# Kernel optimization log

Measured on AMD Instinct MI355X. Metric: run time of the kernel, lower is better.

Reference implementation:

```python
import jax, jax.numpy as jnp
import numpy as np

NQ, NS, QN, SN = 10000, 500, 4, 10   # num_question, num_skill, q/s neighbor sizes
B, S, D = 32, 200, 128               # batch, seq_len, emb_dim
HOPS = 3


def setup_inputs() -> dict:
    key = jax.random.key(0)
    ks = iter(jax.random.split(key, 40))

    def nrm(shape, scale=0.05):
        return jax.random.normal(next(ks), shape, dtype=jnp.float32) * scale

    return {
        "question": jax.random.randint(next(ks), (B, S), 0, NQ),
        "response": jax.random.randint(next(ks), (B, S), 0, 2),
        "mask": jnp.ones((B, S), dtype=jnp.int32),
        "q_neighbors": jax.random.randint(next(ks), (NQ, QN), 0, NS),  # question -> skill ids
        "s_neighbors": jax.random.randint(next(ks), (NS, SN), 0, NQ),  # skill -> question ids
        "qs_skills": jax.random.randint(next(ks), (NQ, 4), 0, NS),     # related skills per question
        "emb_q": nrm((NQ, D), 1.0),
        "emb_s": nrm((NS, D), 1.0),
        "emb_r": nrm((2, D), 1.0),
        "W_ih": nrm((2 * D, 4 * D)), "b_ih": nrm((4 * D,)), "b_hh": nrm((4 * D,)),
        "ft_W": nrm((D, D)), "ft_b": nrm((D,)),
        "agg_W": nrm((HOPS, D, D)), "agg_b": nrm((HOPS, D)),
        "last_W": nrm((D, D)), "last_b": nrm((D,)),
        "q_W": nrm((D, D)), "q_b": nrm((D,)),
        "k_W": nrm((D, D)), "k_b": nrm((D,)),
        "w_W": nrm((2 * D,)), "w_b": nrm(()),
    }


def reference(question, response, mask, q_neighbors, s_neighbors, qs_skills,
              emb_q, emb_s, emb_r, W_ih, b_ih, b_hh, ft_W, ft_b,
              agg_W, agg_b, last_W, last_b, q_W, q_b, k_W, k_b, w_W, w_b):
    # ---- multi-hop GNN aggregation for every (b, t) question (mask == 1 everywhere) ----
    q_flat = question.reshape(-1)              # [B*S]
    lvl1 = q_neighbors[q_flat]                 # [N, QN]            skill ids
    lvl2 = s_neighbors[lvl1]                   # [N, QN, SN]        question ids
    lvl3 = q_neighbors[lvl2]                   # [N, QN, SN, QN]    skill ids
    embs = [emb_q[q_flat], emb_s[lvl1], emb_q[lvl2], emb_s[lvl3]]
    for i in range(HOPS):
        embs = [jnp.tanh((embs[j] + embs[j + 1].mean(axis=-2)) @ agg_W[j] + agg_b[j])
                for j in range(HOPS - i)]
    agg_emb = jnp.tanh(embs[0] @ last_W + last_b).reshape(B, S, D)

    # ---- per-step input + zero-state LSTMCell (source calls lstm_cell without hx) ----
    q_trans = jax.nn.relu(agg_emb @ ft_W + ft_b)
    x = jnp.concatenate([q_trans, emb_r[response]], axis=-1)   # [B, S, 2D]
    gates = x @ W_ih + b_ih + b_hh                             # h_prev = 0, c_prev = 0
    i_g, f_g, g_g, o_g = jnp.split(gates, 4, axis=-1)
    c = jax.nn.sigmoid(i_g) * jnp.tanh(g_g)
    h = jax.nn.sigmoid(o_g) * jnp.tanh(c)                      # [B, S, D]
    states = h[:, :S - 1]                                      # state written at step t

    # ---- soft-recap attention prediction for q_next = question[:, t+1] ----
    q_next = question[:, 1:]                                   # [B, T], T = S-1
    qs = jnp.concatenate([emb_q[q_next][:, :, None, :], emb_s[qs_skills[q_next]]], axis=2)  # [B,T,5,D]

    inner = jnp.einsum('bnd,btmd->btnm', states, qs)           # state/qs inner products
    a_state = (states @ q_W + q_b) @ w_W[:D]                   # [B, N]  MLP_query on states
    a_qs = (qs @ k_W + k_b) @ w_W[D:]                          # [B, T, 5] MLP_key on qs
    logits = a_state[:, None, :, None] + a_qs[:, :, None, :] + w_b  # [B, T, N, 5]

    t_idx = jnp.arange(S - 1)
    valid = t_idx[None, :] <= t_idx[:, None]                   # [T, N]: states 0..t visible at t
    logits = jnp.where(valid[None, :, :, None], logits, -jnp.inf)
    alpha = jax.nn.softmax(logits.reshape(B, S - 1, -1), axis=-1).reshape(logits.shape)
    pred = jnp.sum(alpha * jax.nn.sigmoid(inner), axis=(2, 3))  # [B, T]

    return jnp.zeros((B, S), jnp.float32).at[:, 1:].set(pred)
```

## Files before the change

### kernel.cpp

```cpp
#include <hip/hip_runtime.h>

typedef unsigned short u16;
typedef unsigned int   u32;

#define NQd 10000
#define NSd 500
#define Bd  32
#define Sd  200
#define Td  199
#define Dd  128
#define NR  6368

typedef __attribute__((ext_vector_type(8))) short bf16x8;
typedef __attribute__((ext_vector_type(4))) float f32x4;

__device__ __forceinline__ float sigf(float x) { return 1.f / (1.f + __expf(-x)); }
__device__ __forceinline__ float bf2f(u16 u) { return __uint_as_float(((u32)u) << 16); }
__device__ __forceinline__ u16 f2bf(float f) {
  u32 b = __float_as_uint(f);
  b += 0x7FFFu + ((b >> 16) & 1u);
  return (u16)(b >> 16);
}
__device__ __forceinline__ void unp2(u32 u, float &a, float &b) {
  a = __uint_as_float(u << 16);
  b = __uint_as_float(u & 0xffff0000u);
}
__device__ __forceinline__ void unpack16(uint4 a0, uint4 a1, float* f) {
  unp2(a0.x, f[0], f[1]);  unp2(a0.y, f[2], f[3]);
  unp2(a0.z, f[4], f[5]);  unp2(a0.w, f[6], f[7]);
  unp2(a1.x, f[8], f[9]);  unp2(a1.y, f[10], f[11]);
  unp2(a1.z, f[12], f[13]); unp2(a1.w, f[14], f[15]);
}

struct Args {
  const int *question, *response, *q_nb, *s_nb, *qs_sk;
  const float *emb_q, *emb_s, *emb_r;
  const float *W_ih, *b_ih, *b_hh, *ft_W, *ft_b, *agg_W, *agg_b, *last_W, *last_b;
  const float *q_W, *q_b, *k_W, *k_b, *w_W;
  u16 *tabA, *tabB, *tabC, *tabs1, *tabs2, *G, *states, *embq_bf, *embs_bf, *wts, *wiht;
  float *a_state, *qw, *kw, *scal, *er_part;
  int *qid_map, *resp_map;
};

#define SMEM_U16 21760

__device__ __forceinline__ void mfma_accum(const u16* Al, const u16* Wl,
                                           int l15, int quad, int cw, f32x4 acc[2][2])
{
#pragma unroll
  for (int kc = 0; kc < 4; ++kc) {
    const int ko = kc * 32 + quad * 8;
    bf16x8 af[2], bfv[2];
    af[0]  = *(const bf16x8*)&Al[l15 * 136 + ko];
    af[1]  = *(const bf16x8*)&Al[(16 + l15) * 136 + ko];
    bfv[0] = *(const bf16x8*)&Wl[(cw + l15) * 136 + ko];
    bfv[1] = *(const bf16x8*)&Wl[(cw + 16 + l15) * 136 + ko];
#pragma unroll
    for (int mt = 0; mt < 2; ++mt)
#pragma unroll
      for (int nt = 0; nt < 2; ++nt)
        acc[mt][nt] = __builtin_amdgcn_mfma_f32_16x16x32_bf16(af[mt], bfv[nt], acc[mt][nt], 0, 0, 0);
  }
}

__device__ __forceinline__ void zero_acc(f32x4 acc[2][2]) {
#pragma unroll
  for (int x = 0; x < 2; ++x)
#pragma unroll
    for (int y = 0; y < 2; ++y) acc[x][y] = (f32x4){0.f, 0.f, 0.f, 0.f};
}

__device__ __forceinline__ void stage_A(const u16* Atab, const u16* Btab,
                                        const int* nbr, int K, int tile0, int rows,
                                        int tid, u16* Al)
{
  int r = tid & 31, k0 = (tid >> 5) * 16;
  int row = tile0 + r; if (row >= rows) row = rows - 1;
  const u16* ap = Atab + (long)row * 128 + k0;
  if (K == 0) {
    *(uint4*)&Al[r * 136 + k0]     = *(const uint4*)ap;
    *(uint4*)&Al[r * 136 + k0 + 8] = *(const uint4*)(ap + 8);
  } else {
    float f[16];
    unpack16(*(const uint4*)ap, *(const uint4*)(ap + 8), f);
    float s[16];
#pragma unroll
    for (int q = 0; q < 16; ++q) s[q] = 0.f;
    for (int l = 0; l < K; ++l) {
      int id = nbr[(long)row * K + l];
      const u16* np = Btab + (long)id * 128 + k0;
      float g[16];
      unpack16(*(const uint4*)np, *(const uint4*)(np + 8), g);
#pragma unroll
      for (int q = 0; q < 16; ++q) s[q] += g[q];
    }
    float inv = 1.f / (float)K;
#pragma unroll
    for (int q = 0; q < 16; ++q) f[q] += s[q] * inv;
    u32 p[8];
#pragma unroll
    for (int q = 0; q < 8; ++q)
      p[q] = (u32)f2bf(f[2 * q]) | ((u32)f2bf(f[2 * q + 1]) << 16);
    *(uint4*)&Al[r * 136 + k0]     = make_uint4(p[0], p[1], p[2], p[3]);
    *(uint4*)&Al[r * 136 + k0 + 8] = make_uint4(p[4], p[5], p[6], p[7]);
  }
}

__device__ __forceinline__ void stage_W(const u16* Wt, int tid, u16* Wl)
{
  for (int i = tid; i < 2048; i += 256) {
    int col = i >> 4, seg = i & 15;
    *(uint4*)&Wl[col * 136 + seg * 8] = *(const uint4*)&Wt[(long)col * 128 + seg * 8];
  }
}

__device__ __forceinline__ void gemm_tile(
    const u16* __restrict__ Atab, const u16* __restrict__ Btab,
    const int* __restrict__ nbr, int K,
    const u16* __restrict__ Wt, const float* __restrict__ cbias,
    u16* __restrict__ out, int rows, int tile0, int tid, u16* smem)
{
  u16* Wl = smem;
  u16* Al = smem + 17408;
  stage_W(Wt, tid, Wl);
  stage_A(Atab, Btab, nbr, K, tile0, rows, tid, Al);
  __syncthreads();
  const int lane = tid & 63, wv = tid >> 6;
  const int l15 = lane & 15, quad = lane >> 4, cw = wv * 32;
  f32x4 acc[2][2];
  zero_acc(acc);
  mfma_accum(Al, Wl, l15, quad, cw, acc);
#pragma unroll
  for (int nt = 0; nt < 2; ++nt) {
    int col = cw + nt * 16 + l15;
    float cb = cbias[col];
#pragma unroll
    for (int mt = 0; mt < 2; ++mt) {
      int rbase = tile0 + mt * 16 + quad * 4;
#pragma unroll
      for (int i = 0; i < 4; ++i) {
        int row = rbase + i;
        if (row >= rows) continue;
        out[(long)row * 128 + col] = f2bf(tanhf(acc[mt][nt][i] + cb));
      }
    }
  }
}

__global__ __launch_bounds__(256) void prep_all(Args a)
{
  const int T = gridDim.x * 256;
  for (int i = blockIdx.x * 256 + threadIdx.x; i < 491106; i += T) {
    if (i < 320000) {
      float4 v = *(const float4*)&a.emb_q[(long)i * 4];
      ((uint2*)a.embq_bf)[i] = make_uint2(
          (u32)f2bf(v.x) | ((u32)f2bf(v.y) << 16),
          (u32)f2bf(v.z) | ((u32)f2bf(v.w) << 16));
    } else if (i < 336000) {
      int c = i - 320000;
      float4 v = *(const float4*)&a.emb_s[(long)c * 4];
      ((uint2*)a.embs_bf)[c] = make_uint2(
          (u32)f2bf(v.x) | ((u32)f2bf(v.y) << 16),
          (u32)f2bf(v.z) | ((u32)f2bf(v.w) << 16));
    } else if (i < 417920) {
      int e = i - 336000;
      int seg = e >> 14, r = e & 16383;
      int col = r >> 7, k = r & 127;
      const float* src = (seg < 3) ? (a.agg_W + seg * 16384)
                                   : (seg == 3 ? a.last_W : a.ft_W);
      a.wts[e] = f2bf(src[k * 128 + col]);
    } else if (i < 483456) {
      int e = i - 417920;
      int col = e >> 7, k = e & 127;
      a.wiht[e] = f2bf(a.W_ih[k * 512 + col]);
    } else if (i < 489824) {
      int j = i - 483456;
      int b = j / Td, s = j - b * Td;
      a.qid_map[j]  = a.question[b * Sd + s];
      a.resp_map[j] = a.response[b * Sd + s];
    } else {
      int s = i - 489824;
      if (s < 128) {
        float acc = 0;
        for (int e = 0; e < 128; ++e) acc += a.q_W[s * 128 + e] * a.w_W[e];
        a.qw[s] = acc;
      } else if (s < 256) {
        int d = s - 128; float acc = 0;
        for (int e = 0; e < 128; ++e) acc += a.k_W[d * 128 + e] * a.w_W[128 + e];
        a.kw[d] = acc;
      } else if (s == 256) {
        float acc = 0;
        for (int e = 0; e < 128; ++e) acc += a.q_b[e] * a.w_W[e];
        a.scal[0] = acc;
      } else if (s == 257) {
        float acc = 0;
        for (int e = 0; e < 128; ++e) acc += a.k_b[e] * a.w_W[128 + e];
        a.scal[1] = acc;
      } else {
        int e2 = s - 258, rr = e2 >> 9, col = e2 & 511;
        float acc = a.b_ih[col] + a.b_hh[col];
        for (int d = 0; d < 128; ++d) acc += a.emb_r[rr * Dd + d] * a.W_ih[(128 + d) * 512 + col];
        a.er_part[rr * 512 + col] = acc;
      }
    }
  }
}

__global__ __launch_bounds__(256) void level1(Args a)
{
  __shared__ __align__(16) u16 smem[SMEM_U16];
  const int i = blockIdx.x, tid = threadIdx.x;
  if (i < 313)
    gemm_tile(a.embq_bf, a.embs_bf, a.q_nb, 4, a.wts + 2 * 16384,
              a.agg_b + 256, a.tabA, NQd, i * 32, tid, smem);
  else if (i < 329)
    gemm_tile(a.embs_bf, a.embq_bf, a.s_nb, 10, a.wts + 16384,
              a.agg_b + 128, a.tabs1, NSd, (i - 313) * 32, tid, smem);
  else
    gemm_tile(a.embq_bf, a.embs_bf, a.q_nb, 4, a.wts,
              a.agg_b, a.tabB, NQd, (i - 329) * 32, tid, smem);
}

__global__ __launch_bounds__(256) void level2(Args a)
{
  __shared__ __align__(16) u16 smem[SMEM_U16];
  const int i = blockIdx.x, tid = threadIdx.x;
  if (i < 16)
    gemm_tile(a.tabs1, a.tabA, a.s_nb, 10, a.wts + 16384,
              a.agg_b + 128, a.tabs2, NSd, i * 32, tid, smem);
  else
    gemm_tile(a.tabB, a.tabs1, a.q_nb, 4, a.wts,
              a.agg_b, a.tabC, NQd, (i - 16) * 32, tid, smem);
}

__global__ __launch_bounds__(256) void chain3(Args a)
{
  __shared__ __align__(16) u16 smem[SMEM_U16];
  u16* Wl = smem;
  u16* Al = smem + 17408;
  const int tid = threadIdx.x;
  const int tile0 = blockIdx.x * 32;
  const int lane = tid & 63, wv = tid >> 6;
  const int l15 = lane & 15, quad = lane >> 4, cw = wv * 32;
  f32x4 acc[2][2];

  stage_W(a.wts, tid, Wl);
  stage_A(a.tabC, a.tabs2, a.q_nb, 4, tile0, NQd, tid, Al);
  __syncthreads();
  zero_acc(acc);
  mfma_accum(Al, Wl, l15, quad, cw, acc);
  __syncthreads();
#pragma unroll
  for (int nt = 0; nt < 2; ++nt) {
    int col = cw + nt * 16 + l15;
    float cb = a.agg_b[col];
#pragma unroll
    for (int mt = 0; mt < 2; ++mt)
#pragma unroll
      for (int i = 0; i < 4; ++i) {
        int rL = mt * 16 + quad * 4 + i;
        Al[rL * 136 + col] = f2bf(tanhf(acc[mt][nt][i] + cb));
      }
  }
  stage_W(a.wts + 3 * 16384, tid, Wl);
  __syncthreads();

  zero_acc(acc);
  mfma_accum(Al, Wl, l15, quad, cw, acc);
  __syncthreads();
#pragma unroll
  for (int nt = 0; nt < 2; ++nt) {
    int col = cw + nt * 16 + l15;
    float cb = a.last_b[col];
#pragma unroll
    for (int mt = 0; mt < 2; ++mt)
#pragma unroll
      for (int i = 0; i < 4; ++i) {
        int rL = mt * 16 + quad * 4 + i;
        Al[rL * 136 + col] = f2bf(tanhf(acc[mt][nt][i] + cb));
      }
  }
  stage_W(a.wts + 4 * 16384, tid, Wl);
  __syncthreads();

  zero_acc(acc);
  mfma_accum(Al, Wl, l15, quad, cw, acc);
#pragma unroll
  for (int nt = 0; nt < 2; ++nt) {
    int col = cw + nt * 16 + l15;
    float cb = a.ft_b[col];
#pragma unroll
    for (int mt = 0; mt < 2; ++mt) {
      int rbase = tile0 + mt * 16 + quad * 4;
#pragma unroll
      for (int i = 0; i < 4; ++i) {
        int row = rbase + i;
        if (row >= NQd) continue;
        a.tabA[(long)row * 128 + col] = f2bf(fmaxf(acc[mt][nt][i] + cb, 0.f));
      }
    }
  }
}

__global__ __launch_bounds__(256) void gates_k(Args a)
{
  __shared__ __align__(16) u16 smem[SMEM_U16];
  u16* Wl = smem;
  u16* Al = smem + 17408;
  const int tid = threadIdx.x;
  const int tile0 = blockIdx.x * 32;
  {
    int r = tid & 31, k0 = (tid >> 5) * 16;
    int row = tile0 + r;
    int arow = a.qid_map[row];
    const u16* ap = a.tabA + (long)arow * 128 + k0;
    *(uint4*)&Al[r * 136 + k0]     = *(const uint4*)ap;
    *(uint4*)&Al[r * 136 + k0 + 8] = *(const uint4*)(ap + 8);
  }
  const int lane = tid & 63, wv = tid >> 6;
  const int l15 = lane & 15, quad = lane >> 4, cw = wv * 32;
  f32x4 acc[3][2][2];
  const int goff[3] = {0, 256, 384};
#pragma unroll
  for (int p = 0; p < 3; ++p) {
    __syncthreads();
    stage_W(a.wiht + (long)goff[p] * 128, tid, Wl);
    __syncthreads();
    zero_acc(acc[p]);
    mfma_accum(Al, Wl, l15, quad, cw, acc[p]);
  }
  __syncthreads();
  float* hb = (float*)Wl;
#pragma unroll
  for (int nt = 0; nt < 2; ++nt) {
    int colL = cw + nt * 16 + l15;
#pragma unroll
    for (int mt = 0; mt < 2; ++mt) {
#pragma unroll
      for (int i = 0; i < 4; ++i) {
        int rL = mt * 16 + quad * 4 + i;
        int row = tile0 + rL;
        const float* rb = a.er_part + (long)a.resp_map[row] * 512;
        float iv = acc[0][mt][nt][i] + rb[colL];
        float gv = acc[1][mt][nt][i] + rb[256 + colL];
        float ov = acc[2][mt][nt][i] + rb[384 + colL];
        float c = sigf(iv) * tanhf(gv);
        float h = sigf(ov) * tanhf(c);
        a.states[(long)row * 128 + colL] = f2bf(h);
        hb[rL * 132 + colL] = h;
      }
    }
  }
  __syncthreads();
#pragma unroll
  for (int rr = 0; rr < 8; ++rr) {
    int rL = wv * 8 + rr;
    float p = hb[rL * 132 + lane] * a.qw[lane] + hb[rL * 132 + 64 + lane] * a.qw[64 + lane];
#pragma unroll
    for (int off = 32; off > 0; off >>= 1) p += __shfl_xor(p, off);
    if (lane == 0) a.a_state[tile0 + rL] = p + a.scal[0];
  }
}

__global__ __launch_bounds__(256) void g_k(Args a)
{
  const int n0 = blockIdx.x * 32;
  const int c0 = blockIdx.y * 128;
  const int b  = blockIdx.z;
  int c_hi = c0 + 127; if (c_hi > 994) c_hi = 994;
  if (n0 > c_hi / 5) return;

  __shared__ __align__(16) u16 smem[SMEM_U16];
  u16* Ql = smem;
  u16* Sl = smem + 17408;
  const int tid = threadIdx.x;
  {
    int r = tid & 31, k0 = (tid >> 5) * 16;
    int n = n0 + r; if (n > 198) n = 198;
    const u16* sp = a.states + ((long)b * Td + n) * 128 + k0;
    *(uint4*)&Sl[r * 136 + k0]     = *(const uint4*)sp;
    *(uint4*)&Sl[r * 136 + k0 + 8] = *(const uint4*)(sp + 8);
  }
  {
    int j = tid >> 1, k0 = (tid & 1) * 64;
    int col = c0 + j;
    uint4* dst = (uint4*)&Ql[j * 136 + k0];
    if (col < 995) {
      int t = col / 5, m = col - t * 5;
      int qn = a.question[b * Sd + t + 1];
      const u16* src = (m == 0) ? a.embq_bf + (long)qn * 128
                                : a.embs_bf + (long)a.qs_sk[qn * 4 + (m - 1)] * 128;
      src += k0;
#pragma unroll
      for (int q = 0; q < 8; ++q) dst[q] = ((const uint4*)src)[q];
    } else {
      uint4 z = make_uint4(0, 0, 0, 0);
#pragma unroll
      for (int q = 0; q < 8; ++q) dst[q] = z;
    }
  }
  __syncthreads();
  const int lane = tid & 63, wv = tid >> 6;
  const int l15 = lane & 15, quad = lane >> 4, cw = wv * 32;
  f32x4 acc[2][2];
  zero_acc(acc);
  mfma_accum(Sl, Ql, l15, quad, cw, acc);
#pragma unroll
  for (int nt = 0; nt < 2; ++nt) {
    int col = c0 + cw + nt * 16 + l15;
    if (col >= 995) continue;
#pragma unroll
    for (int mt = 0; mt < 2; ++mt) {
      int nb = n0 + mt * 16 + quad * 4;
      if (nb > 196) continue;
      u32 lo = (u32)f2bf(sigf(acc[mt][nt][0])) | ((u32)f2bf(sigf(acc[mt][nt][1])) << 16);
      u32 hi = (u32)f2bf(sigf(acc[mt][nt][2])) | ((u32)f2bf(sigf(acc[mt][nt][3])) << 16);
      *(uint2*)&a.G[((long)b * 1000 + col) * 200 + nb] = make_uint2(lo, hi);
    }
  }
}

__global__ __launch_bounds__(256) void pred_k(Args a, float* __restrict__ out)
{
  __shared__ float sred[256];
  __shared__ float am[8];
  __shared__ float pmv[8];
  const int item = blockIdx.x;
  const int b = item / Td, t = item - b * Td;
  const int tid = threadIdx.x;

  float v = (tid <= t) ? a.a_state[b * Td + tid] : -1e30f;
  sred[tid] = v; __syncthreads();
  for (int s = 128; s > 0; s >>= 1) { if (tid < s) sred[tid] = fmaxf(sred[tid], sred[tid + s]); __syncthreads(); }
  float amax = sred[0]; __syncthreads();
  float ev = (tid <= t) ? __expf(v - amax) : 0.f;
  sred[tid] = ev; __syncthreads();
  for (int s = 128; s > 0; s >>= 1) { if (tid < s) sred[tid] += sred[tid + s]; __syncthreads(); }
  float Z = sred[0]; __syncthreads();

  int qn = a.question[b * Sd + t + 1];
  if (tid < 160) {
    int m = tid >> 5, j = tid & 31;
    const u16* src = (m == 0) ? a.embq_bf + (long)qn * 128
                              : a.embs_bf + (long)a.qs_sk[qn * 4 + (m - 1)] * 128;
    float p = 0.f;
#pragma unroll
    for (int c = 0; c < 128; c += 32) p += bf2f(src[c + j]) * a.kw[c + j];
#pragma unroll
    for (int off = 16; off > 0; off >>= 1) p += __shfl_xor(p, off);
    if (j == 0) am[m] = p + a.scal[1];
  }
  __syncthreads();
  if (tid == 0) {
    float mx = am[0];
    for (int m = 1; m < 5; ++m) mx = fmaxf(mx, am[m]);
    float e[5], z = 0.f;
    for (int m = 0; m < 5; ++m) { e[m] = __expf(am[m] - mx); z += e[m]; }
    float iz = 1.f / z;
    for (int m = 0; m < 5; ++m) pmv[m] = e[m] * iz;
  }
  __syncthreads();
  float accv = 0.f;
  if (tid <= t) {
    long base = ((long)b * 1000 + (long)t * 5) * 200 + tid;
    accv = ev * (pmv[0] * bf2f(a.G[base])       + pmv[1] * bf2f(a.G[base + 200]) +
                 pmv[2] * bf2f(a.G[base + 400]) + pmv[3] * bf2f(a.G[base + 600]) +
                 pmv[4] * bf2f(a.G[base + 800]));
  }
  sred[tid] = accv; __syncthreads();
  for (int s = 128; s > 0; s >>= 1) { if (tid < s) sred[tid] += sred[tid + s]; __syncthreads(); }
  if (tid == 0) {
    out[b * Sd + t + 1] = sred[0] / Z;
    if (t == 0) out[b * Sd] = 0.f;
  }
}

extern "C" void kernel_launch(void* const* d_in, const int* in_sizes, int n_in,
                              void* d_out, int out_size, void* d_ws, size_t ws_size,
                              hipStream_t stream)
{
  Args a;
  a.question = (const int*)d_in[0];
  a.response = (const int*)d_in[1];
  a.q_nb     = (const int*)d_in[3];
  a.s_nb     = (const int*)d_in[4];
  a.qs_sk    = (const int*)d_in[5];
  a.emb_q    = (const float*)d_in[6];
  a.emb_s    = (const float*)d_in[7];
  a.emb_r    = (const float*)d_in[8];
  a.W_ih     = (const float*)d_in[9];
  a.b_ih     = (const float*)d_in[10];
  a.b_hh     = (const float*)d_in[11];
  a.ft_W     = (const float*)d_in[12];
  a.ft_b     = (const float*)d_in[13];
  a.agg_W    = (const float*)d_in[14];
  a.agg_b    = (const float*)d_in[15];
  a.last_W   = (const float*)d_in[16];
  a.last_b   = (const float*)d_in[17];
  a.q_W      = (const float*)d_in[18];
  a.q_b      = (const float*)d_in[19];
  a.k_W      = (const float*)d_in[20];
  a.k_b      = (const float*)d_in[21];
  a.w_W      = (const float*)d_in[22];

  u16* wsu = (u16*)d_ws;
  const long NT = 1280000, ST = 64000, RT = (long)NR * Dd;
  a.tabA  = wsu;
  a.tabB  = a.tabA + NT;
  a.tabC  = a.tabB + NT;
  a.tabs1 = a.tabC + NT;
  a.tabs2 = a.tabs1 + ST;
  a.G     = wsu;
  a.states  = wsu + 6400000;
  a.embq_bf = a.states + RT;
  a.embs_bf = a.embq_bf + NT;
  a.wts     = a.embs_bf + ST;
  a.wiht    = a.wts + 5 * 16384;
  float* fp = (float*)(a.wiht + 65536);
  a.a_state = fp;
  a.qw      = fp + 6368;
  a.kw      = fp + 6496;
  a.scal    = fp + 6624;
  a.er_part = fp + 6640;
  a.qid_map  = (int*)(fp + 7664);
  a.resp_map = a.qid_map + NR;

  float* out = (float*)d_out;

  prep_all<<<640, 256, 0, stream>>>(a);
  level1<<<642, 256, 0, stream>>>(a);
  level2<<<329, 256, 0, stream>>>(a);
  chain3<<<313, 256, 0, stream>>>(a);
  gates_k<<<199, 256, 0, stream>>>(a);
  g_k<<<dim3(7, 8, Bd), 256, 0, stream>>>(a);
  pred_k<<<NR, 256, 0, stream>>>(a, out);
}
```

Baseline: 205.6 us.

## Fuse sigmoid-gram with prediction reduction, share A tile across level-1 GEMMs

The G matrix of bf16 sigmoids is no longer written to global memory and then re-read by a per-(b,t) prediction kernel. A small per-batch prep kernel now computes the global-max exponentials, prefix normalizers and per-step key softmax weights. The gram kernel then reduces ev*sigmoid*pm directly into per-step accumulators with shared and global atomics, and a tiny finalize kernel writes the output. Level-1 GEMMs that share the same gathered A tile are merged into one block, and tanhf/sigmoid use fast rcp-based approximations. Risks include atomic ordering nondeterminism, numerics from using a global max instead of a per-prefix max, and approximate tanh.

```diff
diff --git a/kernel.cpp b/kernel.cpp
--- a/kernel.cpp
+++ b/kernel.cpp
@@ -10,11 +10,20 @@
 #define Td  199
 #define Dd  128
 #define NR  6368
+#define PB  208
 
 typedef __attribute__((ext_vector_type(8))) short bf16x8;
 typedef __attribute__((ext_vector_type(4))) float f32x4;
 
-__device__ __forceinline__ float sigf(float x) { return 1.f / (1.f + __expf(-x)); }
+__device__ __forceinline__ float sigf(float x) {
+  return __builtin_amdgcn_rcpf(1.f + __expf(-x));
+}
+__device__ __forceinline__ float tanh_f(float x) {
+  float ax = fminf(fabsf(x), 15.f);
+  float e = __expf(2.f * ax);
+  float r = 1.f - 2.f * __builtin_amdgcn_rcpf(e + 1.f);
+  return copysignf(r, x);
+}
 __device__ __forceinline__ float bf2f(u16 u) { return __uint_as_float(((u32)u) << 16); }
 __device__ __forceinline__ u16 f2bf(float f) {
   u32 b = __float_as_uint(f);
@@ -37,8 +46,8 @@
   const float *emb_q, *emb_s, *emb_r;
   const float *W_ih, *b_ih, *b_hh, *ft_W, *ft_b, *agg_W, *agg_b, *last_W, *last_b;
   const float *q_W, *q_b, *k_W, *k_b, *w_W;
-  u16 *tabA, *tabB, *tabC, *tabs1, *tabs2, *G, *states, *embq_bf, *embs_bf, *wts, *wiht;
-  float *a_state, *qw, *kw, *scal, *er_part;
+  u16 *tabA, *tabB, *tabC, *tabs1, *tabs2, *states, *embq_bf, *embs_bf, *wts, *wiht;
+  float *a_state, *qw, *kw, *scal, *er_part, *ev, *invZ, *pred_acc, *pm;
   int *qid_map, *resp_map;
 };
 
@@ -114,6 +123,27 @@
   }
 }
 
+__device__ __forceinline__ void epi_tanh_global(const f32x4 acc[2][2], const float* cbias,
+                                                u16* out, int rows, int tile0,
+                                                int l15, int quad, int cw)
+{
+#pragma unroll
+  for (int nt = 0; nt < 2; ++nt) {
+    int col = cw + nt * 16 + l15;
+    float cb = cbias[col];
+#pragma unroll
+    for (int mt = 0; mt < 2; ++mt) {
+      int rbase = tile0 + mt * 16 + quad * 4;
+#pragma unroll
+      for (int i = 0; i < 4; ++i) {
+        int row = rbase + i;
+        if (row >= rows) continue;
+        out[(long)row * 128 + col] = f2bf(tanh_f(acc[mt][nt][i] + cb));
+      }
+    }
+  }
+}
+
 __device__ __forceinline__ void gemm_tile(
     const u16* __restrict__ Atab, const u16* __restrict__ Btab,
     const int* __restrict__ nbr, int K,
@@ -130,21 +160,7 @@
   f32x4 acc[2][2];
   zero_acc(acc);
   mfma_accum(Al, Wl, l15, quad, cw, acc);
-#pragma unroll
-  for (int nt = 0; nt < 2; ++nt) {
-    int col = cw + nt * 16 + l15;
-    float cb = cbias[col];
-#pragma unroll
-    for (int mt = 0; mt < 2; ++mt) {
-      int rbase = tile0 + mt * 16 + quad * 4;
-#pragma unroll
-      for (int i = 0; i < 4; ++i) {
-        int row = rbase + i;
-        if (row >= rows) continue;
-        out[(long)row * 128 + col] = f2bf(tanhf(acc[mt][nt][i] + cb));
-      }
-    }
-  }
+  epi_tanh_global(acc, cbias, out, rows, tile0, l15, quad, cw);
 }
 
 __global__ __launch_bounds__(256) void prep_all(Args a)
@@ -206,19 +222,33 @@
   }
 }
 
-__global__ __launch_bounds__(256) void level1(Args a)
+__global__ __launch_bounds__(256) void level1m(Args a)
 {
   __shared__ __align__(16) u16 smem[SMEM_U16];
   const int i = blockIdx.x, tid = threadIdx.x;
-  if (i < 313)
-    gemm_tile(a.embq_bf, a.embs_bf, a.q_nb, 4, a.wts + 2 * 16384,
-              a.agg_b + 256, a.tabA, NQd, i * 32, tid, smem);
-  else if (i < 329)
+  if (i >= 313) {
     gemm_tile(a.embs_bf, a.embq_bf, a.s_nb, 10, a.wts + 16384,
               a.agg_b + 128, a.tabs1, NSd, (i - 313) * 32, tid, smem);
-  else
-    gemm_tile(a.embq_bf, a.embs_bf, a.q_nb, 4, a.wts,
-              a.agg_b, a.tabB, NQd, (i - 329) * 32, tid, smem);
+    return;
+  }
+  u16* Wl = smem;
+  u16* Al = smem + 17408;
+  const int tile0 = i * 32;
+  const int lane = tid & 63, wv = tid >> 6;
+  const int l15 = lane & 15, quad = lane >> 4, cw = wv * 32;
+  f32x4 acc[2][2];
+  stage_W(a.wts + 2 * 16384, tid, Wl);
+  stage_A(a.embq_bf, a.embs_bf, a.q_nb, 4, tile0, NQd, tid, Al);
+  __syncthreads();
+  zero_acc(acc);
+  mfma_accum(Al, Wl, l15, quad, cw, acc);
+  epi_tanh_global(acc, a.agg_b + 256, a.tabA, NQd, tile0, l15, quad, cw);
+  __syncthreads();
+  stage_W(a.wts, tid, Wl);
+  __syncthreads();
+  zero_acc(acc);
+  mfma_accum(Al, Wl, l15, quad, cw, acc);
+  epi_tanh_global(acc, a.agg_b, a.tabB, NQd, tile0, l15, quad, cw);
 }
 
 __global__ __launch_bounds__(256) void level2(Args a)
@@ -259,7 +289,7 @@
 #pragma unroll
       for (int i = 0; i < 4; ++i) {
         int rL = mt * 16 + quad * 4 + i;
-        Al[rL * 136 + col] = f2bf(tanhf(acc[mt][nt][i] + cb));
+        Al[rL * 136 + col] = f2bf(tanh_f(acc[mt][nt][i] + cb));
       }
   }
   stage_W(a.wts + 3 * 16384, tid, Wl);
@@ -277,7 +307,7 @@
 #pragma unroll
       for (int i = 0; i < 4; ++i) {
         int rL = mt * 16 + quad * 4 + i;
-        Al[rL * 136 + col] = f2bf(tanhf(acc[mt][nt][i] + cb));
+        Al[rL * 136 + col] = f2bf(tanh_f(acc[mt][nt][i] + cb));
       }
   }
   stage_W(a.wts + 4 * 16384, tid, Wl);
@@ -344,8 +374,8 @@
         float iv = acc[0][mt][nt][i] + rb[colL];
         float gv = acc[1][mt][nt][i] + rb[256 + colL];
         float ov = acc[2][mt][nt][i] + rb[384 + colL];
-        float c = sigf(iv) * tanhf(gv);
-        float h = sigf(ov) * tanhf(c);
+        float c = sigf(iv) * tanh_f(gv);
+        float h = sigf(ov) * tanh_f(c);
         a.states[(long)row * 128 + colL] = f2bf(h);
         hb[rL * 132 + colL] = h;
       }
@@ -362,18 +392,69 @@
   }
 }
 
-__global__ __launch_bounds__(256) void g_k(Args a)
+__global__ __launch_bounds__(256) void bprep(Args a)
+{
+  __shared__ float red[256];
+  __shared__ float evl[256];
+  __shared__ float kwl[128];
+  const int b = blockIdx.x, tid = threadIdx.x;
+  if (tid < 128) kwl[tid] = a.kw[tid];
+  float v = (tid < Td) ? a.a_state[b * Td + tid] : -1e30f;
+  red[tid] = v; __syncthreads();
+  for (int s = 128; s > 0; s >>= 1) { if (tid < s) red[tid] = fmaxf(red[tid], red[tid + s]); __syncthreads(); }
+  float gmax = red[0];
+  float e = (tid < Td) ? __expf(v - gmax) : 0.f;
+  evl[tid] = e;
+  if (tid < Td) { a.ev[b * PB + tid] = e; a.pred_acc[b * PB + tid] = 0.f; }
+  __syncthreads();
+  if (tid < Td) {
+    float Z = 0.f;
+    for (int n = 0; n <= tid; ++n) Z += evl[n];
+    a.invZ[b * PB + tid] = 1.f / Z;
+    int qn = a.question[b * Sd + tid + 1];
+    float am[5];
+#pragma unroll
+    for (int m = 0; m < 5; ++m) {
+      const u16* src = (m == 0) ? a.embq_bf + (long)qn * 128
+                                : a.embs_bf + (long)a.qs_sk[qn * 4 + (m - 1)] * 128;
+      float s = 0.f;
+      for (int k = 0; k < 128; k += 8) {
+        uint4 u = *(const uint4*)&src[k];
+        float f[8];
+        unp2(u.x, f[0], f[1]); unp2(u.y, f[2], f[3]);
+        unp2(u.z, f[4], f[5]); unp2(u.w, f[6], f[7]);
+#pragma unroll
+        for (int q = 0; q < 8; ++q) s = fmaf(f[q], kwl[k + q], s);
+      }
+      am[m] = s + a.scal[1];
+    }
+    float mx = am[0];
+#pragma unroll
+    for (int m = 1; m < 5; ++m) mx = fmaxf(mx, am[m]);
+    float ex[5], z = 0.f;
+#pragma unroll
+    for (int m = 0; m < 5; ++m) { ex[m] = __expf(am[m] - mx); z += ex[m]; }
+    float iz = 1.f / z;
+#pragma unroll
+    for (int m = 0; m < 5; ++m) a.pm[((long)b * PB + tid) * 5 + m] = ex[m] * iz;
+  }
+}
+
+__global__ __launch_bounds__(256) void gk_pred(Args a)
 {
   const int n0 = blockIdx.x * 32;
   const int c0 = blockIdx.y * 128;
   const int b  = blockIdx.z;
   int c_hi = c0 + 127; if (c_hi > 994) c_hi = 994;
-  if (n0 > c_hi / 5) return;
+  const int tmax = c_hi / 5, tmin = c0 / 5;
+  if (n0 > tmax) return;
 
   __shared__ __align__(16) u16 smem[SMEM_U16];
+  __shared__ float predl[32];
   u16* Ql = smem;
   u16* Sl = smem + 17408;
   const int tid = threadIdx.x;
+  if (tid < 32) predl[tid] = 0.f;
   {
     int r = tid & 31, k0 = (tid >> 5) * 16;
     int n = n0 + r; if (n > 198) n = 198;
@@ -405,74 +486,44 @@
   f32x4 acc[2][2];
   zero_acc(acc);
   mfma_accum(Sl, Ql, l15, quad, cw, acc);
+
 #pragma unroll
   for (int nt = 0; nt < 2; ++nt) {
     int col = c0 + cw + nt * 16 + l15;
     if (col >= 995) continue;
+    int t = col / 5, m = col - t * 5;
+    float pmv = a.pm[((long)b * PB + t) * 5 + m];
+    float part = 0.f;
 #pragma unroll
     for (int mt = 0; mt < 2; ++mt) {
       int nb = n0 + mt * 16 + quad * 4;
-      if (nb > 196) continue;
-      u32 lo = (u32)f2bf(sigf(acc[mt][nt][0])) | ((u32)f2bf(sigf(acc[mt][nt][1])) << 16);
-      u32 hi = (u32)f2bf(sigf(acc[mt][nt][2])) | ((u32)f2bf(sigf(acc[mt][nt][3])) << 16);
-      *(uint2*)&a.G[((long)b * 1000 + col) * 200 + nb] = make_uint2(lo, hi);
-    }
-  }
-}
-
-__global__ __launch_bounds__(256) void pred_k(Args a, float* __restrict__ out)
-{
-  __shared__ float sred[256];
-  __shared__ float am[8];
-  __shared__ float pmv[8];
-  const int item = blockIdx.x;
-  const int b = item / Td, t = item - b * Td;
-  const int tid = threadIdx.x;
-
-  float v = (tid <= t) ? a.a_state[b * Td + tid] : -1e30f;
-  sred[tid] = v; __syncthreads();
-  for (int s = 128; s > 0; s >>= 1) { if (tid < s) sred[tid] = fmaxf(sred[tid], sred[tid + s]); __syncthreads(); }
-  float amax = sred[0]; __syncthreads();
-  float ev = (tid <= t) ? __expf(v - amax) : 0.f;
-  sred[tid] = ev; __syncthreads();
-  for (int s = 128; s > 0; s >>= 1) { if (tid < s) sred[tid] += sred[tid + s]; __syncthreads(); }
-  float Z = sred[0]; __syncthreads();
-
-  int qn = a.question[b * Sd + t + 1];
-  if (tid < 160) {
-    int m = tid >> 5, j = tid & 31;
-    const u16* src = (m == 0) ? a.embq_bf + (long)qn * 128
-                              : a.embs_bf + (long)a.qs_sk[qn * 4 + (m - 1)] * 128;
-    float p = 0.f;
-#pragma unroll
-    for (int c = 0; c < 128; c += 32) p += bf2f(src[c + j]) * a.kw[c + j];
-#pragma unroll
-    for (int off = 16; off > 0; off >>= 1) p += __shfl_xor(p, off);
-    if (j == 0) am[m] = p + a.scal[1];
-  }
-  __syncthreads();
-  if (tid == 0) {
-    float mx = am[0];
-    for (int m = 1; m < 5; ++m) mx = fmaxf(mx, am[m]);
-    float e[5], z = 0.f;
-    for (int m = 0; m < 5; ++m) { e[m] = __expf(am[m] - mx); z += e[m]; }
-    float iz = 1.f / z;
-    for (int m = 0; m < 5; ++m) pmv[m] = e[m] * iz;
-  }
-  __syncthreads();
-  float accv = 0.f;
-  if (tid <= t) {
-    long base = ((long)b * 1000 + (long)t * 5) * 200 + tid;
-    accv = ev * (pmv[0] * bf2f(a.G[base])       + pmv[1] * bf2f(a.G[base + 200]) +
-                 pmv[2] * bf2f(a.G[base + 400]) + pmv[3] * bf2f(a.G[base + 600]) +
-                 pmv[4] * bf2f(a.G[base + 800]));
-  }
-  sred[tid] = accv; __syncthreads();
-  for (int s = 128; s > 0; s >>= 1) { if (tid < s) sred[tid] += sred[tid + s]; __syncthreads(); }
-  if (tid == 0) {
-    out[b * Sd + t + 1] = sred[0] / Z;
-    if (t == 0) out[b * Sd] = 0.f;
-  }
+      if (nb > t) continue;
+      float4 ev4 = *(const float4*)&a.ev[b * PB + nb];
+      float evv[4] = {ev4.x, ev4.y, ev4.z, ev4.w};
+#pragma unroll
+      for (int i = 0; i < 4; ++i) {
+        int n = nb + i;
+        if (n > t || n > 198) continue;
+        part += evv[i] * sigf(acc[mt][nt][i]);
+      }
+    }
+    part *= pmv;
+    if (part != 0.f) atomicAdd(&predl[t - tmin], part);
+  }
+  __syncthreads();
+  const int tcnt = tmax - tmin + 1;
+  if (tid < tcnt) {
+    float pv = predl[tid];
+    if (pv != 0.f) atomicAdd(&a.pred_acc[b * PB + tmin + tid], pv);
+  }
+}
+
+__global__ __launch_bounds__(256) void finalize(Args a, float* __restrict__ out)
+{
+  int i = blockIdx.x * 256 + threadIdx.x;
+  if (i >= Bd * Sd) return;
+  int b = i / Sd, s = i - b * Sd;
+  out[i] = (s == 0) ? 0.f : a.pred_acc[b * PB + s - 1] * a.invZ[b * PB + s - 1];
 }
 
 extern "C" void kernel_launch(void* const* d_in, const int* in_sizes, int n_in,
@@ -510,8 +561,7 @@
   a.tabC  = a.tabB + NT;
   a.tabs1 = a.tabC + NT;
   a.tabs2 = a.tabs1 + ST;
-  a.G     = wsu;
-  a.states  = wsu + 6400000;
+  a.states  = a.tabs2 + ST;
   a.embq_bf = a.states + RT;
   a.embs_bf = a.embq_bf + NT;
   a.wts     = a.embs_bf + ST;
@@ -522,16 +572,21 @@
   a.kw      = fp + 6496;
   a.scal    = fp + 6624;
   a.er_part = fp + 6640;
-  a.qid_map  = (int*)(fp + 7664);
+  a.ev       = fp + 7664;
+  a.invZ     = a.ev + 32 * PB;
+  a.pred_acc = a.invZ + 32 * PB;
+  a.pm       = a.pred_acc + 32 * PB;
+  a.qid_map  = (int*)(a.pm + 32 * PB * 5);
   a.resp_map = a.qid_map + NR;
 
   float* out = (float*)d_out;
 
   prep_all<<<640, 256, 0, stream>>>(a);
-  level1<<<642, 256, 0, stream>>>(a);
+  level1m<<<329, 256, 0, stream>>>(a);
   level2<<<329, 256, 0, stream>>>(a);
   chain3<<<313, 256, 0, stream>>>(a);
   gates_k<<<199, 256, 0, stream>>>(a);
-  g_k<<<dim3(7, 8, Bd), 256, 0, stream>>>(a);
-  pred_k<<<NR, 256, 0, stream>>>(a, out);
-}
+  bprep<<<Bd, 256, 0, stream>>>(a);
+  gk_pred<<<dim3(7, 8, Bd), 256, 0, stream>>>(a);
+  finalize<<<25, 256, 0, stream>>>(a, out);
+}
```

After: 196.7 us. -4.3%, faster.
